# Kernel optimization log

Hardware: AMD Instinct MI355X
Metric: run time of the kernel (lower is better)

Reference implementation:

```python
import jax, jax.numpy as jnp
import numpy as np

PATCH = 64      # patch_size
K = 16          # num_patches
UNF_K = 16      # unfold kernel
UNF_S = 8       # unfold stride


def setup_inputs() -> dict:
    key = jax.random.key(0)
    k0, k1, k2 = jax.random.split(key, 3)
    B, C, H, W = 32, 3, 384, 384
    x = jax.random.normal(k0, (B, C, H, W), dtype=jnp.float32)
    # encoder params: Conv2d(3,32,3,s2,p1) -> ReLU -> Conv2d(32,64,3,s2,p1) -> GAP
    w1 = jax.random.normal(k1, (32, 3, 3, 3), dtype=jnp.float32) * 0.1
    b1 = jnp.zeros((32,), dtype=jnp.float32)
    w2 = jax.random.normal(k2, (64, 32, 3, 3), dtype=jnp.float32) * 0.05
    b2 = jnp.zeros((64,), dtype=jnp.float32)
    return {"x": x, "w1": w1, "b1": b1, "w2": w2, "b2": b2}


def _patch_variances(x):
    # torch.var(unfold(x,16,8), dim=1), unbiased, over C*16*16 = 768 elems.
    # Computed via window sums instead of materializing the unfold tensor.
    win = (1, 1, UNF_K, UNF_K)
    st = (1, 1, UNF_S, UNF_S)
    s = jax.lax.reduce_window(x, 0.0, jax.lax.add, win, st, 'VALID')
    s2 = jax.lax.reduce_window(x * x, 0.0, jax.lax.add, win, st, 'VALID')
    s = s.sum(axis=1)    # [B, gh, gw]
    s2 = s2.sum(axis=1)  # [B, gh, gw]
    n = x.shape[1] * UNF_K * UNF_K  # 768
    var = (s2 - s * s / n) / (n - 1)
    return var.reshape(var.shape[0], -1)  # [B, gh*gw], row-major like F.unfold


def _encode(patches, w1, b1, w2, b2):
    # patches: [N, 3, 64, 64] -> [N, 64]
    dn = ('NCHW', 'OIHW', 'NCHW')
    y = jax.lax.conv_general_dilated(patches, w1, (2, 2), [(1, 1), (1, 1)],
                                     dimension_numbers=dn) + b1[None, :, None, None]
    y = jax.nn.relu(y)
    y = jax.lax.conv_general_dilated(y, w2, (2, 2), [(1, 1), (1, 1)],
                                     dimension_numbers=dn) + b2[None, :, None, None]
    return y.mean(axis=(2, 3))  # AdaptiveAvgPool2d(1)


def reference(x, w1, b1, w2, b2):
    B, C, H, W = x.shape
    var = _patch_variances(x)                 # [B, L]
    _, idx = jax.lax.top_k(var, K)            # [B, K]
    # faithful (buggy) decode from the source: divisor is W//8, step 8
    h = (idx // (W // UNF_S)) * UNF_S         # [B, K]
    w = (idx % (W // UNF_S)) * UNF_S          # [B, K]

    def slice_one(img, hh, ww):
        # dynamic_slice clamps starts so the 64x64 crop stays in-bounds
        return jax.lax.dynamic_slice(img, (0, hh, ww), (C, PATCH, PATCH))

    gather = jax.vmap(lambda img, hs, ws: jax.vmap(
        lambda hh, ww: slice_one(img, hh, ww))(hs, ws))
    patches = gather(x, h, w)                 # [B, K, 3, 64, 64]
    feats = _encode(patches.reshape(B * K, C, PATCH, PATCH), w1, b1, w2, b2)
    return feats.reshape(B, K, -1).mean(axis=1)  # [B, 64]
```

## Files before the change

kernel.cpp:

```cpp
#include <hip/hip_runtime.h>
#include <math.h>

#define NB 32
#define GH 47
#define GW 47
#define NWIN (GH*GW)
#define KSEL 16
#define RPITCH 17
#define SEG 48

__global__ __launch_bounds__(256) void k_var(const float* __restrict__ x,
                                             float* __restrict__ var)
{
    __shared__ double hs [3][24][SEG];
    __shared__ double hs2[3][24][SEG];
    int gyp = blockIdx.x;
    int b   = blockIdx.y;
    int tid = threadIdx.x;
    int R0  = gyp * 16;

    for (int tau = tid; tau < 3*24*SEG; tau += 256) {
        int sg = tau % SEG;
        int t2 = tau / SEG;
        int rr = t2 % 24;
        int c  = t2 / 24;
        int row = R0 + rr;
        double s = 0.0, s2 = 0.0;
        if (row < 384) {
            const float* px = x + (((size_t)(b*3 + c)*384 + row)*384 + sg*8);
            #pragma unroll
            for (int q = 0; q < 2; ++q) {
                float4 v = *reinterpret_cast<const float4*>(px + q*4);
                double a0 = v.x, a1 = v.y, a2 = v.z, a3 = v.w;
                s  += a0 + a1 + a2 + a3;
                s2 = fma(a0,a0, fma(a1,a1, fma(a2,a2, fma(a3,a3, s2))));
            }
        }
        hs [c][rr][sg] = s;
        hs2[c][rr][sg] = s2;
    }
    __syncthreads();

    if (tid < 188) {
        int which = tid & 1;
        int rest  = tid >> 1;
        int gx = rest % 47, g = rest / 47;
        int gy = gyp*2 + g;
        if (gy < GH) {
            const double* base = which ? &hs2[0][0][0] : &hs[0][0][0];
            double S = 0.0;
            #pragma unroll
            for (int c = 0; c < 3; ++c)
                #pragma unroll
                for (int r = 0; r < 16; ++r) {
                    const double* rp = base + ((c*24) + (g*8 + r))*SEG + gx;
                    S += rp[0] + rp[1];
                }
            double P = __shfl_xor(S, 1, 64);
            if (which == 0) {
                var[(size_t)b*NWIN + gy*GW + gx] =
                    (float)((P - S*S/768.0) / 767.0);
            }
        }
    }
}

__global__ void k_sel(const float* __restrict__ var, int* __restrict__ coords)
{
    int b = blockIdx.x, l = threadIdx.x;
    unsigned long long key[35];
    #pragma unroll
    for (int j = 0; j < 35; ++j) {
        int idx = j*64 + l;
        unsigned long long kk = 0ULL;
        if (idx < NWIN) {
            unsigned u = __float_as_uint(var[(size_t)b*NWIN + idx]);
            unsigned mono = u ^ ((unsigned)((int)u >> 31) | 0x80000000u);
            kk = ((unsigned long long)mono << 12) | (unsigned)(4095 - idx);
        }
        key[j] = kk;
    }
    for (int it = 0; it < KSEL; ++it) {
        unsigned long long bk = 0ULL;
        #pragma unroll
        for (int j = 0; j < 35; ++j) bk = key[j] > bk ? key[j] : bk;
        #pragma unroll
        for (int m = 1; m < 64; m <<= 1) {
            unsigned long long o = __shfl_xor(bk, m, 64);
            bk = o > bk ? o : bk;
        }
        #pragma unroll
        for (int j = 0; j < 35; ++j) if (key[j] == bk) key[j] = 0ULL;
        if (l == 0) {
            int idx = 4095 - (int)(bk & 0xFFFULL);
            int h = (idx / 48) * 8; if (h > 320) h = 320;
            int w = (idx % 48) * 8; if (w > 320) w = 320;
            coords[(b*KSEL + it)*2 + 0] = h;
            coords[(b*KSEL + it)*2 + 1] = w;
        }
    }
}

__global__ __launch_bounds__(512, 2) void k_encode(const float* __restrict__ x,
    const float* __restrict__ w1, const float* __restrict__ b1,
    const int* __restrict__ coords, float* __restrict__ sbuf)
{
    __shared__ float4 sin4[3*66*RPITCH];
    __shared__ float  s_part[8][2][8][3];
    __shared__ float  s_c31[4][8][3];

    int p    = blockIdx.x;
    int bimg = p >> 4;
    int tid  = threadIdx.x;
    int h0 = coords[p*2 + 0];
    int w0 = coords[p*2 + 1];

    float* sinf = (float*)sin4;

    if (tid < 243) {
        int c = tid / 81, j = tid - c*81;
        if (j < 17) {
            sin4[(c*66 + 0)*RPITCH + j] = make_float4(0.f, 0.f, 0.f, 0.f);
        } else {
            int r  = j - 16;
            int sw = (r >> 1) & 7;
            sinf[((c*66 + r)*RPITCH + sw)*4] = 0.f;
        }
    }

    #pragma unroll
    for (int it = 0; it < 6; ++it) {
        int fi  = tid + it*512;
        int c   = fi >> 10;
        int rem = fi & 1023;
        int y   = rem >> 4;
        int x4  = rem & 15;
        float4 v = *reinterpret_cast<const float4*>(
            x + (((size_t)(bimg*3 + c)*384 + (h0 + y))*384 + w0 + x4*4));
        int r  = y + 1;
        int sw = (r >> 1) & 7;
        float vals[4] = {v.x, v.y, v.z, v.w};
        #pragma unroll
        for (int e = 0; e < 4; ++e) {
            int pcol = x4*4 + 1 + e;
            int k  = pcol >> 2, bb = pcol & 3;
            int ks = (k < 16) ? ((k & 8) | ((k & 7) ^ sw)) : 16;
            sinf[((c*66 + r)*RPITCH + ks)*4 + bb] = vals[e];
        }
    }
    __syncthreads();

    int wave = tid >> 6;
    int lane = tid & 63;
    int sub  = wave & 1;
    int icg  = __builtin_amdgcn_readfirstlane(tid >> 7);
    int iy   = sub*16 + (lane >> 2);
    int xq   = lane & 3;

    float acc[8][8];
    #pragma unroll
    for (int i = 0; i < 8; ++i)
        #pragma unroll
        for (int u = 0; u < 8; ++u) acc[i][u] = 0.f;

    const float* w1g = w1 + icg*8*27;

    for (int ch = 0; ch < 3; ++ch) {
        for (int ky = 0; ky < 3; ++ky) {
            int r    = 2*iy + ky;
            int sw   = (r >> 1) & 7;
            int base = (ch*66 + r)*RPITCH;
            float s[17];
            #pragma unroll
            for (int j = 0; j < 4; ++j) {
                int k = 4*xq + j;
                float4 v = sin4[base + ((k & 8) | ((k & 7) ^ sw))];
                s[4*j+0] = v.x; s[4*j+1] = v.y; s[4*j+2] = v.z; s[4*j+3] = v.w;
            }
            {
                int k  = 4*xq + 4;
                int ks = (k < 16) ? ((k & 8) | ((k & 7) ^ sw)) : 16;
                s[16] = sinf[(base + ks)*4];
            }
            const float* wp = w1g + ch*9 + ky*3;
            #pragma unroll
            for (int i = 0; i < 8; ++i) {
                float wA = wp[i*27 + 0];
                float wB = wp[i*27 + 1];
                float wC = wp[i*27 + 2];
                #pragma unroll
                for (int u = 0; u < 8; ++u)
                    acc[i][u] = fmaf(s[2*u], wA,
                                 fmaf(s[2*u+1], wB,
                                  fmaf(s[2*u+2], wC, acc[i][u])));
            }
        }
    }

    float R[8][3];
    #pragma unroll
    for (int i = 0; i < 8; ++i) {
        float bias = b1[icg*8 + i];
        float c1 = 0.f, c2 = 0.f, v7 = 0.f;
        #pragma unroll
        for (int u = 0; u < 8; ++u) {
            float v = fmaxf(acc[i][u] + bias, 0.f);
            if (u & 1) c2 += v; else c1 += v;
            if (u == 7) v7 = v;
        }
        R[i][0] = c2 - ((xq == 3) ? v7 : 0.f);
        R[i][1] = c1;
        R[i][2] = c2;
    }

    #pragma unroll
    for (int m = 1; m <= 2; m <<= 1)
        #pragma unroll
        for (int i = 0; i < 8; ++i)
            #pragma unroll
            for (int k = 0; k < 3; ++k)
                R[i][k] += __shfl_xor(R[i][k], m, 64);

    float c31[8][3];
    #pragma unroll
    for (int i = 0; i < 8; ++i)
        #pragma unroll
        for (int k = 0; k < 3; ++k)
            c31[i][k] = __shfl(R[i][k], 60, 64);

    #pragma unroll
    for (int m = 8; m < 64; m <<= 1)
        #pragma unroll
        for (int i = 0; i < 8; ++i)
            #pragma unroll
            for (int k = 0; k < 3; ++k)
                R[i][k] += __shfl_xor(R[i][k], m, 64);

    if (lane == 0) {
        #pragma unroll
        for (int i = 0; i < 8; ++i)
            #pragma unroll
            for (int k = 0; k < 3; ++k)
                s_part[wave][0][i][k] = R[i][k];
    } else if (lane == 4) {
        #pragma unroll
        for (int i = 0; i < 8; ++i)
            #pragma unroll
            for (int k = 0; k < 3; ++k)
                s_part[wave][1][i][k] = R[i][k];
    }
    if (sub == 1 && lane == 8) {
        #pragma unroll
        for (int i = 0; i < 8; ++i)
            #pragma unroll
            for (int k = 0; k < 3; ++k)
                s_c31[icg][i][k] = c31[i][k];
    }
    __syncthreads();

    if (tid < 288) {
        int ic = tid / 9, j = tid - ic*9;
        int ky = j / 3, kx = j - ky*3;
        int g = ic >> 3, i = ic & 7;
        float even = s_part[2*g][0][i][kx] + s_part[2*g+1][0][i][kx];
        float odd  = s_part[2*g][1][i][kx] + s_part[2*g+1][1][i][kx];
        float val = (ky == 1) ? even : odd;
        if (ky == 0) val = odd - s_c31[g][i][kx];
        sbuf[(size_t)p*288 + tid] = val;
    }
}

__global__ __launch_bounds__(256) void k_reduce(const float* __restrict__ sbuf,
    const float* __restrict__ w2, const float* __restrict__ b2,
    float* __restrict__ out)
{
    __shared__ float Ssum[288];
    __shared__ float s_part[256];
    int b = blockIdx.x, tid = threadIdx.x;

    for (int i = tid; i < 288; i += 256) {
        float s = 0.f;
        #pragma unroll
        for (int k = 0; k < KSEL; ++k)
            s += sbuf[(size_t)(b*KSEL + k)*288 + i];
        Ssum[i] = s;
    }
    __syncthreads();

    int oc = tid & 63, q = tid >> 6;
    const float4* w4 = reinterpret_cast<const float4*>(w2 + oc*288 + q*72);
    const float4* S4 = reinterpret_cast<const float4*>(Ssum + q*72);
    float a = 0.f;
    #pragma unroll
    for (int t = 0; t < 18; ++t) {
        float4 wv = w4[t];
        float4 sv = S4[t];
        a = fmaf(wv.x, sv.x, fmaf(wv.y, sv.y,
             fmaf(wv.z, sv.z, fmaf(wv.w, sv.w, a))));
    }
    s_part[tid] = a;
    __syncthreads();
    if (tid < 64) {
        float t = s_part[tid] + s_part[64 + tid] + s_part[128 + tid] + s_part[192 + tid];
        out[b*64 + tid] = b2[tid] + t * (1.0f/4096.0f);
    }
}

extern "C" void kernel_launch(void* const* d_in, const int* in_sizes, int n_in,
                              void* d_out, int out_size, void* d_ws, size_t ws_size,
                              hipStream_t stream)
{
    const float* x  = (const float*)d_in[0];
    const float* w1 = (const float*)d_in[1];
    const float* b1 = (const float*)d_in[2];
    const float* w2 = (const float*)d_in[3];
    const float* b2 = (const float*)d_in[4];
    float* out = (float*)d_out;

    char* ws = (char*)d_ws;
    int*   coords = (int*)ws;
    float* var    = (float*)(ws + 4096);
    float* sbuf   = (float*)(ws + 287744);

    k_var   <<<dim3(24, NB), 256, 0, stream>>>(x, var);
    k_sel   <<<NB,            64, 0, stream>>>(var, coords);
    k_encode<<<NB*KSEL,      512, 0, stream>>>(x, w1, b1, coords, sbuf);
    k_reduce<<<NB,           256, 0, stream>>>(sbuf, w2, b2, out);
}
```

Before: 74.11 us.

## Rewrite top-k with shared-memory block argmax and widen encode to 1024 threads

Replaces the single-wave 64-bit key top-k with a 256-thread block kernel that stages the variances in LDS and runs 16 rounds of block-wide argmax, breaking ties toward the lower index. The first-conv encode kernel now uses 1024 threads per patch, each wave computing 4 output channels instead of 8, which halves accumulator registers and doubles the waves per block. The top-k rounds now need two block barriers each, and occupancy of the 1024-thread blocks depends on register and LDS limits.

```diff
diff --git a/kernel.cpp b/kernel.cpp
--- a/kernel.cpp
+++ b/kernel.cpp
@@ -65,49 +65,63 @@
     }
 }
 
-__global__ void k_sel(const float* __restrict__ var, int* __restrict__ coords)
-{
-    int b = blockIdx.x, l = threadIdx.x;
-    unsigned long long key[35];
-    #pragma unroll
-    for (int j = 0; j < 35; ++j) {
-        int idx = j*64 + l;
-        unsigned long long kk = 0ULL;
-        if (idx < NWIN) {
-            unsigned u = __float_as_uint(var[(size_t)b*NWIN + idx]);
-            unsigned mono = u ^ ((unsigned)((int)u >> 31) | 0x80000000u);
-            kk = ((unsigned long long)mono << 12) | (unsigned)(4095 - idx);
-        }
-        key[j] = kk;
-    }
-    for (int it = 0; it < KSEL; ++it) {
-        unsigned long long bk = 0ULL;
-        #pragma unroll
-        for (int j = 0; j < 35; ++j) bk = key[j] > bk ? key[j] : bk;
+__global__ __launch_bounds__(256) void k_topk(const float* __restrict__ var,
+                                              int* __restrict__ coords)
+{
+    __shared__ float lv[NWIN];
+    __shared__ float s_val[4];
+    __shared__ int   s_idx[4];
+    __shared__ int   chosen[KSEL];
+    int b = blockIdx.x, tid = threadIdx.x;
+    int lane = tid & 63, wavid = tid >> 6;
+
+    for (int i = tid; i < NWIN; i += 256) lv[i] = var[(size_t)b*NWIN + i];
+    __syncthreads();
+
+    for (int k = 0; k < KSEL; ++k) {
+        float bv = -INFINITY; int bi = NWIN;
+        for (int i = tid; i < NWIN; i += 256) {
+            float v = lv[i];
+            if (v > bv) { bv = v; bi = i; }
+        }
         #pragma unroll
         for (int m = 1; m < 64; m <<= 1) {
-            unsigned long long o = __shfl_xor(bk, m, 64);
-            bk = o > bk ? o : bk;
-        }
-        #pragma unroll
-        for (int j = 0; j < 35; ++j) if (key[j] == bk) key[j] = 0ULL;
-        if (l == 0) {
-            int idx = 4095 - (int)(bk & 0xFFFULL);
-            int h = (idx / 48) * 8; if (h > 320) h = 320;
-            int w = (idx % 48) * 8; if (w > 320) w = 320;
-            coords[(b*KSEL + it)*2 + 0] = h;
-            coords[(b*KSEL + it)*2 + 1] = w;
-        }
-    }
-}
-
-__global__ __launch_bounds__(512, 2) void k_encode(const float* __restrict__ x,
+            float ov = __shfl_xor(bv, m, 64);
+            int   oi = __shfl_xor(bi, m, 64);
+            if (ov > bv || (ov == bv && oi < bi)) { bv = ov; bi = oi; }
+        }
+        if (lane == 0) { s_val[wavid] = bv; s_idx[wavid] = bi; }
+        __syncthreads();
+        if (tid == 0) {
+            float cv = s_val[0]; int ci = s_idx[0];
+            #pragma unroll
+            for (int wv = 1; wv < 4; ++wv) {
+                if (s_val[wv] > cv || (s_val[wv] == cv && s_idx[wv] < ci)) {
+                    cv = s_val[wv]; ci = s_idx[wv];
+                }
+            }
+            chosen[k] = ci;
+            lv[ci] = -INFINITY;
+        }
+        __syncthreads();
+    }
+
+    if (tid < KSEL) {
+        int idx = chosen[tid];
+        int h = (idx / 48) * 8; if (h > 320) h = 320;
+        int w = (idx % 48) * 8; if (w > 320) w = 320;
+        coords[(b*KSEL + tid)*2 + 0] = h;
+        coords[(b*KSEL + tid)*2 + 1] = w;
+    }
+}
+
+__global__ __launch_bounds__(1024, 1) void k_encode(const float* __restrict__ x,
     const float* __restrict__ w1, const float* __restrict__ b1,
     const int* __restrict__ coords, float* __restrict__ sbuf)
 {
     __shared__ float4 sin4[3*66*RPITCH];
-    __shared__ float  s_part[8][2][8][3];
-    __shared__ float  s_c31[4][8][3];
+    __shared__ float  s_part[16][2][4][3];
+    __shared__ float  s_c31[8][4][3];
 
     int p    = blockIdx.x;
     int bimg = p >> 4;
@@ -129,8 +143,8 @@
     }
 
     #pragma unroll
-    for (int it = 0; it < 6; ++it) {
-        int fi  = tid + it*512;
+    for (int it = 0; it < 3; ++it) {
+        int fi  = tid + it*1024;
         int c   = fi >> 10;
         int rem = fi & 1023;
         int y   = rem >> 4;
@@ -153,17 +167,17 @@
     int wave = tid >> 6;
     int lane = tid & 63;
     int sub  = wave & 1;
-    int icg  = __builtin_amdgcn_readfirstlane(tid >> 7);
+    int icq  = __builtin_amdgcn_readfirstlane(tid >> 7);
     int iy   = sub*16 + (lane >> 2);
     int xq   = lane & 3;
 
-    float acc[8][8];
-    #pragma unroll
-    for (int i = 0; i < 8; ++i)
+    float acc[4][8];
+    #pragma unroll
+    for (int i = 0; i < 4; ++i)
         #pragma unroll
         for (int u = 0; u < 8; ++u) acc[i][u] = 0.f;
 
-    const float* w1g = w1 + icg*8*27;
+    const float* w1g = w1 + icq*4*27;
 
     for (int ch = 0; ch < 3; ++ch) {
         for (int ky = 0; ky < 3; ++ky) {
@@ -184,7 +198,7 @@
             }
             const float* wp = w1g + ch*9 + ky*3;
             #pragma unroll
-            for (int i = 0; i < 8; ++i) {
+            for (int i = 0; i < 4; ++i) {
                 float wA = wp[i*27 + 0];
                 float wB = wp[i*27 + 1];
                 float wC = wp[i*27 + 2];
@@ -197,10 +211,10 @@
         }
     }
 
-    float R[8][3];
-    #pragma unroll
-    for (int i = 0; i < 8; ++i) {
-        float bias = b1[icg*8 + i];
+    float R[4][3];
+    #pragma unroll
+    for (int i = 0; i < 4; ++i) {
+        float bias = b1[icq*4 + i];
         float c1 = 0.f, c2 = 0.f, v7 = 0.f;
         #pragma unroll
         for (int u = 0; u < 8; ++u) {
@@ -216,14 +230,14 @@
     #pragma unroll
     for (int m = 1; m <= 2; m <<= 1)
         #pragma unroll
-        for (int i = 0; i < 8; ++i)
+        for (int i = 0; i < 4; ++i)
             #pragma unroll
             for (int k = 0; k < 3; ++k)
                 R[i][k] += __shfl_xor(R[i][k], m, 64);
 
-    float c31[8][3];
-    #pragma unroll
-    for (int i = 0; i < 8; ++i)
+    float c31[4][3];
+    #pragma unroll
+    for (int i = 0; i < 4; ++i)
         #pragma unroll
         for (int k = 0; k < 3; ++k)
             c31[i][k] = __shfl(R[i][k], 60, 64);
@@ -231,37 +245,37 @@
     #pragma unroll
     for (int m = 8; m < 64; m <<= 1)
         #pragma unroll
-        for (int i = 0; i < 8; ++i)
+        for (int i = 0; i < 4; ++i)
             #pragma unroll
             for (int k = 0; k < 3; ++k)
                 R[i][k] += __shfl_xor(R[i][k], m, 64);
 
     if (lane == 0) {
         #pragma unroll
-        for (int i = 0; i < 8; ++i)
+        for (int i = 0; i < 4; ++i)
             #pragma unroll
             for (int k = 0; k < 3; ++k)
                 s_part[wave][0][i][k] = R[i][k];
     } else if (lane == 4) {
         #pragma unroll
-        for (int i = 0; i < 8; ++i)
+        for (int i = 0; i < 4; ++i)
             #pragma unroll
             for (int k = 0; k < 3; ++k)
                 s_part[wave][1][i][k] = R[i][k];
     }
     if (sub == 1 && lane == 8) {
         #pragma unroll
-        for (int i = 0; i < 8; ++i)
-            #pragma unroll
-            for (int k = 0; k < 3; ++k)
-                s_c31[icg][i][k] = c31[i][k];
+        for (int i = 0; i < 4; ++i)
+            #pragma unroll
+            for (int k = 0; k < 3; ++k)
+                s_c31[icq][i][k] = c31[i][k];
     }
     __syncthreads();
 
     if (tid < 288) {
         int ic = tid / 9, j = tid - ic*9;
         int ky = j / 3, kx = j - ky*3;
-        int g = ic >> 3, i = ic & 7;
+        int g = ic >> 2, i = ic & 3;
         float even = s_part[2*g][0][i][kx] + s_part[2*g+1][0][i][kx];
         float odd  = s_part[2*g][1][i][kx] + s_part[2*g+1][1][i][kx];
         float val = (ky == 1) ? even : odd;
@@ -323,7 +337,7 @@
     float* sbuf   = (float*)(ws + 287744);
 
     k_var   <<<dim3(24, NB), 256, 0, stream>>>(x, var);
-    k_sel   <<<NB,            64, 0, stream>>>(var, coords);
-    k_encode<<<NB*KSEL,      512, 0, stream>>>(x, w1, b1, coords, sbuf);
+    k_topk  <<<NB,           256, 0, stream>>>(var, coords);
+    k_encode<<<NB*KSEL,     1024, 0, stream>>>(x, w1, b1, coords, sbuf);
     k_reduce<<<NB,           256, 0, stream>>>(sbuf, w2, b2, out);
 }
```

New measurement: 77.30 us. 1.04x slower.
